# Kernel tuning notes

Hardware: AMD Instinct MI355X
Metric: run time of the kernel (lower is better)

The kernel has to match this reference:

```python
import jax, jax.numpy as jnp
import numpy as np

TEMP = float(np.e)

def _normalize(v):
    n = jnp.linalg.norm(v, axis=-1, keepdims=True)
    return v / jnp.maximum(n, 1e-12)

def setup_inputs() -> dict:
    key = jax.random.key(0)
    ks = jax.random.split(key, 18)
    N, D, H, O, E = 8192, 1024, 2048, 1024, 8
    s = 0.02
    return {
        "x": jax.random.normal(ks[0], (N, D), jnp.float32),
        "gate_w": jax.random.normal(ks[1], (D, E), jnp.float32) * s,
        "gate_b": jnp.zeros((E,), jnp.float32),
        "ph_w1": jax.random.normal(ks[2], (D, 32), jnp.float32) * s,
        "ph_b1": jnp.zeros((32,), jnp.float32),
        "ph_w2": jax.random.normal(ks[3], (32, 16), jnp.float32) * s,
        "ph_b2": jnp.zeros((16,), jnp.float32),
        "cl_w1": jax.random.normal(ks[4], (D, 16), jnp.float32) * s,
        "cl_b1": jnp.zeros((16,), jnp.float32),
        "cl_w2": jax.random.normal(ks[5], (16, 1), jnp.float32) * s,
        "cl_b2": jnp.zeros((1,), jnp.float32),
        "sigs": jax.random.normal(ks[6], (E, 16), jnp.float32) * 0.1,
        "e_w1": jax.random.normal(ks[7], (E, D, H), jnp.float32) * s,
        "e_b1": jnp.zeros((E, H), jnp.float32),
        "e_w2": jax.random.normal(ks[8], (E, H, O), jnp.float32) * s,
        "e_b2": jnp.zeros((E, O), jnp.float32),
    }

def reference(x, gate_w, gate_b, ph_w1, ph_b1, ph_w2, ph_b2,
              cl_w1, cl_b1, cl_w2, cl_b2, sigs, e_w1, e_b1, e_w2, e_b2):
    E = sigs.shape[0]
    # gating
    scores = (x @ gate_w + gate_b) / TEMP            # [N, E]
    probs = jax.nn.softmax(scores, axis=-1)
    # ph signature matching
    ph_feat = _normalize(jax.nn.relu(x @ ph_w1 + ph_b1) @ ph_w2 + ph_b2)  # [N, 16]
    sig_n = _normalize(sigs)                          # [E, 16]
    ph_match = (ph_feat @ sig_n.T + 1.0) / 2.0        # [N, E]
    effective = probs * ph_match
    # data-dependent k (torch uses .item(); here traced int used only in mask compare)
    clarity = jax.nn.sigmoid(jax.nn.relu(x @ cl_w1 + cl_b1) @ cl_w2 + cl_b2)  # [N,1]
    n_active = E - clarity[:, 0] * (E - 2)
    k = jnp.clip(jnp.floor(n_active.mean() + 0.5).astype(jnp.int32), 2, E)
    # rank-based top-k mask (jit-compatible for traced k)
    ranks = jnp.argsort(jnp.argsort(-effective, axis=-1), axis=-1)  # [N, E]
    mask = (ranks < k).astype(effective.dtype)
    weights = effective * mask
    weights = weights / (weights.sum(axis=-1, keepdims=True) + 1e-8)
    # load-balance loss
    f = (weights > 0).astype(probs.dtype).mean(axis=0)
    P = probs.mean(axis=0)
    lb_loss = 0.01 * E * (f * P).sum()
    # dense all-expert MLP (dropout is identity at eval)
    h = jax.nn.relu(jnp.einsum('nd,edh->neh', x, e_w1) + e_b1)   # [N, E, H]
    outs = jnp.einsum('neh,eho->neo', h, e_w2) + e_b2            # [N, E, O]
    y = jnp.einsum('ne,neo->no', weights, outs)                   # [N, O]
    return y, lb_loss
```

## Files before the change

kernel.cpp:

```cpp
#include <hip/hip_runtime.h>
#include <hip/hip_bf16.h>
#include <stdint.h>

typedef __attribute__((ext_vector_type(8))) _Float16 half8;
typedef __attribute__((ext_vector_type(4))) float f32x4;
typedef __attribute__((ext_vector_type(4))) unsigned short us4;
typedef __attribute__((ext_vector_type(8))) unsigned short us8;
typedef __attribute__((ext_vector_type(4))) int i32x4;

#define N_TOK 8192
#define DIM   1024
#define HDIM  2048
#define ODIM  1024

__device__ __forceinline__ unsigned short f2h(float f) {
  _Float16 h = (_Float16)f;
  union { _Float16 h; unsigned short u; } c; c.h = h; return c.u;
}

__device__ __forceinline__ void gload_lds16(const void* g, void* l) {
  __builtin_amdgcn_global_load_lds(
      (const __attribute__((address_space(1))) unsigned int*)g,
      (__attribute__((address_space(3))) unsigned int*)l, 16, 0, 0);
}

template <int EPI>
__global__ __launch_bounds__(256) void gemm_kernel(
    const unsigned short* __restrict__ A, const unsigned short* __restrict__ B,
    int N, int K,
    const float* __restrict__ bias, unsigned short* __restrict__ Hout,
    const float* __restrict__ Wg, int e, float* __restrict__ Y,
    const int* __restrict__ lst, const int* __restrict__ cntTrue,
    const int* __restrict__ cntPad)
{
  __shared__ half8 ldsA[2][512];
  __shared__ half8 ldsB[2][512];
  const int lane = threadIdx.x & 63, wid = threadIdx.x >> 6;
  const int wr = wid >> 1, wc = wid & 1;

  const int nwg = gridDim.x * gridDim.y;
  const int orig = blockIdx.y * gridDim.x + blockIdx.x;
  const int qq = nwg >> 3;
  const int swz = (orig & 7) * qq + (orig >> 3);
  const int bx = swz % gridDim.x, by = swz / gridDim.x;
  const int rowbase = by * 128, colbase = bx * 128;

  const int padc = cntPad[e];
  if (rowbase >= padc) return;

  int rG0 = rowbase + lane, rG1 = rowbase + 64 + lane;
  if (EPI == 1) { rG0 = lst[rG0]; rG1 = lst[rG1]; }

  f32x4 acc[4][4];
#pragma unroll
  for (int m = 0; m < 4; ++m)
#pragma unroll
    for (int n = 0; n < 4; ++n) acc[m][n] = f32x4{0.f, 0.f, 0.f, 0.f};

  auto stage = [&](int buf, int ktile) {
#pragma unroll
    for (int i = 0; i < 4; ++i) {
      const int c = wid * 4 + i;
      const int cc = c & 7, kq = cc >> 1, half = cc & 1;
      const int koff = ktile * 32 + kq * 8;
      if (c < 8) {
        const int arow = half ? rG1 : rG0;
        gload_lds16(A + (size_t)arow * K + koff,
                    &ldsA[buf][kq * 128 + half * 64]);
      } else {
        gload_lds16(B + (size_t)(colbase + half * 64 + lane) * K + koff,
                    &ldsB[buf][kq * 128 + half * 64]);
      }
    }
  };

  const int KT = K >> 5;
  stage(0, 0);
  for (int kt = 0; kt < KT; ++kt) {
    const int buf = kt & 1;
    __syncthreads();
    if (kt + 1 < KT) stage(buf ^ 1, kt + 1);

    half8 af[4], bfr[4];
    const int kqo = (lane >> 4) * 128;
    const int rA = wr * 64 + (lane & 15);
    const int rB = wc * 64 + (lane & 15);
#pragma unroll
    for (int m = 0; m < 4; ++m) af[m] = ldsA[buf][kqo + rA + m * 16];
#pragma unroll
    for (int n = 0; n < 4; ++n) bfr[n] = ldsB[buf][kqo + rB + n * 16];
#pragma unroll
    for (int m = 0; m < 4; ++m)
#pragma unroll
      for (int n = 0; n < 4; ++n)
        acc[m][n] = __builtin_amdgcn_mfma_f32_16x16x32_f16(af[m], bfr[n], acc[m][n], 0, 0, 0);
  }

  const int r0 = rowbase + wr * 64, c0 = colbase + wc * 64;
  if (EPI == 1) {
#pragma unroll
    for (int n = 0; n < 4; ++n) {
      const int col = c0 + n * 16 + (lane & 15);
      const float bv = bias[col];
#pragma unroll
      for (int m = 0; m < 4; ++m)
#pragma unroll
        for (int r = 0; r < 4; ++r) {
          const int slot = r0 + m * 16 + (lane >> 4) * 4 + r;
          float v = acc[m][n][r] + bv;
          v = v > 0.f ? v : 0.f;
          Hout[(size_t)slot * N + col] = f2h(v);
        }
    }
  } else {
    const int cntT = cntTrue[e];
#pragma unroll
    for (int m = 0; m < 4; ++m) {
      const int sbase = r0 + m * 16 + (lane >> 4) * 4;
      const i32x4 og = *(const i32x4*)&lst[sbase];
#pragma unroll
      for (int r = 0; r < 4; ++r) {
        const int slot = sbase + r;
        if (slot < cntT) {
          const int otok = og[r];
          const float wv = Wg[otok * 8 + e];
#pragma unroll
          for (int n = 0; n < 4; ++n) {
            const int col = c0 + n * 16 + (lane & 15);
            Y[(size_t)otok * ODIM + col] += wv * acc[m][n][r];
          }
        }
      }
    }
  }
}

__global__ __launch_bounds__(256) void gating_kernel(
    const float* __restrict__ x,
    const float* __restrict__ gate_w, const float* __restrict__ gate_b,
    const float* __restrict__ ph_w1, const float* __restrict__ ph_b1,
    const float* __restrict__ ph_w2, const float* __restrict__ ph_b2,
    const float* __restrict__ cl_w1, const float* __restrict__ cl_b1,
    const float* __restrict__ cl_w2, const float* __restrict__ cl_b2,
    const float* __restrict__ sigs,
    unsigned short* __restrict__ xh,
    float* __restrict__ eff_o,
    float* __restrict__ pclar, float* __restrict__ pP)
{
  const int lane = threadIdx.x & 63, wid = threadIdx.x >> 6;
  const int tok = blockIdx.x * 4 + wid;

  float g[8], p1[32], c1[16];
#pragma unroll
  for (int i = 0; i < 8; ++i) g[i] = 0.f;
#pragma unroll
  for (int i = 0; i < 32; ++i) p1[i] = 0.f;
#pragma unroll
  for (int i = 0; i < 16; ++i) c1[i] = 0.f;

  const f32x4* x4 = (const f32x4*)(x + (size_t)tok * DIM);
  us4* xh4 = (us4*)(xh + (size_t)tok * DIM);
#pragma unroll
  for (int d0 = 0; d0 < 4; ++d0) {
    const f32x4 xv = x4[d0 * 64 + lane];
    us4 ov;
#pragma unroll
    for (int j = 0; j < 4; ++j) {
      const int d = (d0 * 64 + lane) * 4 + j;
      const float xd = xv[j];
      ov[j] = f2h(xd);
      const f32x4* gw = (const f32x4*)(gate_w + d * 8);
#pragma unroll
      for (int q = 0; q < 2; ++q) { const f32x4 w = gw[q];
#pragma unroll
        for (int r = 0; r < 4; ++r) g[q * 4 + r] += xd * w[r]; }
      const f32x4* pw = (const f32x4*)(ph_w1 + d * 32);
#pragma unroll
      for (int q = 0; q < 8; ++q) { const f32x4 w = pw[q];
#pragma unroll
        for (int r = 0; r < 4; ++r) p1[q * 4 + r] += xd * w[r]; }
      const f32x4* cw = (const f32x4*)(cl_w1 + d * 16);
#pragma unroll
      for (int q = 0; q < 4; ++q) { const f32x4 w = cw[q];
#pragma unroll
        for (int r = 0; r < 4; ++r) c1[q * 4 + r] += xd * w[r]; }
    }
    xh4[d0 * 64 + lane] = ov;
  }
#pragma unroll
  for (int i = 0; i < 8; ++i)
#pragma unroll
    for (int s = 0; s < 6; ++s) g[i] += __shfl_xor(g[i], 1 << s);
#pragma unroll
  for (int i = 0; i < 32; ++i)
#pragma unroll
    for (int s = 0; s < 6; ++s) p1[i] += __shfl_xor(p1[i], 1 << s);
#pragma unroll
  for (int i = 0; i < 16; ++i)
#pragma unroll
    for (int s = 0; s < 6; ++s) c1[i] += __shfl_xor(c1[i], 1 << s);

  float sc[8]; float mx = -1e30f;
#pragma unroll
  for (int k = 0; k < 8; ++k) { sc[k] = (g[k] + gate_b[k]) / 2.718281828459045f; mx = fmaxf(mx, sc[k]); }
  float ex[8]; float sum = 0.f;
#pragma unroll
  for (int k = 0; k < 8; ++k) { ex[k] = expf(sc[k] - mx); sum += ex[k]; }
  float pe[8];
#pragma unroll
  for (int k = 0; k < 8; ++k) pe[k] = ex[k] / sum;

  float rh[32];
#pragma unroll
  for (int h = 0; h < 32; ++h) { const float v = p1[h] + ph_b1[h]; rh[h] = v > 0.f ? v : 0.f; }
  float feat[16];
#pragma unroll
  for (int q = 0; q < 16; ++q) {
    float f = ph_b2[q];
#pragma unroll
    for (int h = 0; h < 32; ++h) f += rh[h] * ph_w2[h * 16 + q];
    feat[q] = f;
  }
  float nn = 0.f;
#pragma unroll
  for (int q = 0; q < 16; ++q) nn += feat[q] * feat[q];
  const float den = fmaxf(sqrtf(nn), 1e-12f);
#pragma unroll
  for (int q = 0; q < 16; ++q) feat[q] = feat[q] / den;

  float eff[8];
#pragma unroll
  for (int k = 0; k < 8; ++k) {
    float s2 = 0.f;
#pragma unroll
    for (int q = 0; q < 16; ++q) { const float sv = sigs[k * 16 + q]; s2 += sv * sv; }
    const float sden = fmaxf(sqrtf(s2), 1e-12f);
    float dot = 0.f;
#pragma unroll
    for (int q = 0; q < 16; ++q) dot += feat[q] * (sigs[k * 16 + q] / sden);
    eff[k] = pe[k] * ((dot + 1.0f) / 2.0f);
  }

  float z = cl_b2[0];
#pragma unroll
  for (int c = 0; c < 16; ++c) { float v = c1[c] + cl_b1[c]; v = v > 0.f ? v : 0.f; z += v * cl_w2[c]; }
  const float clar = 1.0f / (1.0f + expf(-z));

  if (lane == 0) {
#pragma unroll
    for (int k = 0; k < 8; ++k) eff_o[tok * 8 + k] = eff[k];
  }
  __shared__ float shc[4];
  __shared__ float shP[4][8];
  if (lane == 0) { shc[wid] = clar;
#pragma unroll
    for (int k = 0; k < 8; ++k) shP[wid][k] = pe[k]; }
  __syncthreads();
  if (threadIdx.x == 0) {
    pclar[blockIdx.x] = shc[0] + shc[1] + shc[2] + shc[3];
#pragma unroll
    for (int k = 0; k < 8; ++k)
      pP[blockIdx.x * 8 + k] = shP[0][k] + shP[1][k] + shP[2][k] + shP[3][k];
  }
}

__global__ void zero_kernel(int* __restrict__ gcount) {
  if (threadIdx.x < 8) gcount[threadIdx.x] = 0;
}

__global__ __launch_bounds__(256) void weights_kernel(
    const float* __restrict__ eff_i, const float* __restrict__ pclar,
    float* __restrict__ wout, int* __restrict__ f_part,
    int* __restrict__ gcount, int* __restrict__ lst)
{
  __shared__ float red[256];
  __shared__ int cnt[8];
  __shared__ int ksh;
  const int tid = threadIdx.x;
  float s = 0.f;
  for (int i = tid; i < 2048; i += 256) s += pclar[i];
  red[tid] = s; __syncthreads();
  for (int off = 128; off > 0; off >>= 1) { if (tid < off) red[tid] += red[tid + off]; __syncthreads(); }
  if (tid == 0) {
    const float mean_na = 8.0f - 6.0f * (red[0] / 8192.0f);
    int k = (int)floorf(mean_na + 0.5f);
    ksh = k < 2 ? 2 : (k > 8 ? 8 : k);
  }
  if (tid < 8) cnt[tid] = 0;
  __syncthreads();
  const int k = ksh;
  const int t = blockIdx.x * 256 + tid;
  const f32x4* ep = (const f32x4*)(eff_i + t * 8);
  const f32x4 ea = ep[0], eb = ep[1];
  const float ef[8] = {ea[0], ea[1], ea[2], ea[3], eb[0], eb[1], eb[2], eb[3]};
  float w[8]; float wsum = 0.f; int act[8];
#pragma unroll
  for (int e2 = 0; e2 < 8; ++e2) {
    int r = 0;
#pragma unroll
    for (int j = 0; j < 8; ++j) r += (int)((ef[j] > ef[e2]) || ((j < e2) && (ef[j] == ef[e2])));
    const float we = (r < k) ? ef[e2] : 0.f;
    w[e2] = we; wsum += we; act[e2] = we > 0.f ? 1 : 0;
  }
  const float dn = wsum + 1e-8f;
#pragma unroll
  for (int e2 = 0; e2 < 8; ++e2) wout[t * 8 + e2] = w[e2] / dn;
#pragma unroll
  for (int e2 = 0; e2 < 8; ++e2)
    if (act[e2]) {
      atomicAdd(&cnt[e2], 1);
      const int p = atomicAdd(&gcount[e2], 1);
      lst[e2 * N_TOK + p] = t;
    }
  __syncthreads();
  if (tid < 8) f_part[blockIdx.x * 8 + tid] = cnt[tid];
}

__global__ __launch_bounds__(256) void pad_kernel(
    const int* __restrict__ gcount, int* __restrict__ gpad, int* __restrict__ lst)
{
  const int tid = threadIdx.x;
  for (int e2 = 0; e2 < 8; ++e2) {
    const int a = gcount[e2];
    const int pc = (a + 127) & ~127;
    if (tid == 0) gpad[e2] = pc;
    if (a > 0) {
      const int last = lst[e2 * N_TOK + a - 1];
      for (int i = a + tid; i < pc; i += 256) lst[e2 * N_TOK + i] = last;
    }
  }
}

__global__ __launch_bounds__(256) void lb_kernel(
    const float* __restrict__ pP, const int* __restrict__ f_part, float* __restrict__ lbout)
{
  __shared__ float red[256];
  __shared__ float Ps[8], Fs[8];
  const int tid = threadIdx.x;
  for (int e2 = 0; e2 < 8; ++e2) {
    float s = 0.f;
    for (int i = tid; i < 2048; i += 256) s += pP[i * 8 + e2];
    red[tid] = s; __syncthreads();
    for (int off = 128; off > 0; off >>= 1) { if (tid < off) red[tid] += red[tid + off]; __syncthreads(); }
    if (tid == 0) Ps[e2] = red[0];
    __syncthreads();
    red[tid] = (tid < 32) ? (float)f_part[tid * 8 + e2] : 0.f;
    __syncthreads();
    for (int off = 128; off > 0; off >>= 1) { if (tid < off) red[tid] += red[tid + off]; __syncthreads(); }
    if (tid == 0) Fs[e2] = red[0];
    __syncthreads();
  }
  if (tid == 0) {
    float lb = 0.f;
    for (int e2 = 0; e2 < 8; ++e2) lb += (Fs[e2] / 8192.0f) * (Ps[e2] / 8192.0f);
    lbout[0] = 0.01f * 8.0f * lb;
  }
}

__global__ __launch_bounds__(256) void yinit_kernel(
    const float* __restrict__ w, const float* __restrict__ b2, float* __restrict__ y)
{
  const int idx = blockIdx.x * 256 + threadIdx.x;
  const int n = idx >> 8, o4 = idx & 255;
  const f32x4* bv = (const f32x4*)b2;
  f32x4 a = f32x4{0.f, 0.f, 0.f, 0.f};
  const float* wr = w + n * 8;
#pragma unroll
  for (int e2 = 0; e2 < 8; ++e2) a += wr[e2] * bv[e2 * 256 + o4];
  ((f32x4*)y)[idx] = a;
}

__global__ __launch_bounds__(256) void transpose_kernel(
    const float* __restrict__ in, unsigned short* __restrict__ out, int R, int C)
{
  __shared__ __align__(16) unsigned short tb[64][72];
  const float* ip = in + (size_t)blockIdx.z * R * C;
  unsigned short* op = out + (size_t)blockIdx.z * R * C;
  const int r0 = blockIdx.y * 64, c0 = blockIdx.x * 64;
  const int tr = threadIdx.x >> 4, tc4 = (threadIdx.x & 15) * 4;
#pragma unroll
  for (int i = 0; i < 4; ++i) {
    const int rr = tr + i * 16;
    const f32x4 v = *(const f32x4*)(ip + (size_t)(r0 + rr) * C + c0 + tc4);
#pragma unroll
    for (int j = 0; j < 4; ++j) tb[tc4 + j][rr] = f2h(v[j]);
  }
  __syncthreads();
  const int oc = threadIdx.x >> 3, or8 = (threadIdx.x & 7) * 8;
#pragma unroll
  for (int i = 0; i < 2; ++i) {
    const int c = oc + i * 32;
    const us8 v = *(const us8*)&tb[c][or8];
    *(us8*)(op + (size_t)(c0 + c) * R + r0 + or8) = v;
  }
}

extern "C" void kernel_launch(void* const* d_in, const int* in_sizes, int n_in,
                              void* d_out, int out_size, void* d_ws, size_t ws_size,
                              hipStream_t stream)
{
  const float* x      = (const float*)d_in[0];
  const float* gate_w = (const float*)d_in[1];
  const float* gate_b = (const float*)d_in[2];
  const float* ph_w1  = (const float*)d_in[3];
  const float* ph_b1  = (const float*)d_in[4];
  const float* ph_w2  = (const float*)d_in[5];
  const float* ph_b2  = (const float*)d_in[6];
  const float* cl_w1  = (const float*)d_in[7];
  const float* cl_b1  = (const float*)d_in[8];
  const float* cl_w2  = (const float*)d_in[9];
  const float* cl_b2  = (const float*)d_in[10];
  const float* sigs   = (const float*)d_in[11];
  const float* e_w1   = (const float*)d_in[12];
  const float* e_b1   = (const float*)d_in[13];
  const float* e_w2   = (const float*)d_in[14];
  const float* e_b2   = (const float*)d_in[15];
  float* y = (float*)d_out;
  char* ws = (char*)d_ws;

  float* eff    = (float*)(ws + 0);
  float* wts    = (float*)(ws + 262144);
  float* pclar  = (float*)(ws + 524288);
  float* pP     = (float*)(ws + 532480);
  int*   f_part = (int*)(ws + 598016);
  int*   gcount = (int*)(ws + 599040);
  int*   gpad   = (int*)(ws + 599072);
  int*   lst    = (int*)(ws + 655360);
  unsigned short* xh  = (unsigned short*)(ws + 1048576);
  unsigned short* W1T = (unsigned short*)(ws + 17825792u);
  unsigned short* W2T = (unsigned short*)(ws + 51380224u);
  unsigned short* Hh  = (unsigned short*)(ws + 84934656u);

  transpose_kernel<<<dim3(32, 16, 8), 256, 0, stream>>>(e_w1, W1T, 1024, 2048);
  transpose_kernel<<<dim3(16, 32, 8), 256, 0, stream>>>(e_w2, W2T, 2048, 1024);
  gating_kernel<<<2048, 256, 0, stream>>>(x, gate_w, gate_b, ph_w1, ph_b1, ph_w2, ph_b2,
                                          cl_w1, cl_b1, cl_w2, cl_b2, sigs,
                                          xh, eff, pclar, pP);
  zero_kernel<<<1, 64, 0, stream>>>(gcount);
  weights_kernel<<<32, 256, 0, stream>>>(eff, pclar, wts, f_part, gcount, lst);
  pad_kernel<<<1, 256, 0, stream>>>(gcount, gpad, lst);
  lb_kernel<<<1, 256, 0, stream>>>(pP, f_part, y + (size_t)N_TOK * ODIM);
  yinit_kernel<<<8192, 256, 0, stream>>>(wts, e_b2, y);

  for (int e2 = 0; e2 < 8; ++e2) {
    gemm_kernel<1><<<dim3(16, 64), 256, 0, stream>>>(
        xh, W1T + (size_t)e2 * HDIM * DIM, HDIM, DIM,
        e_b1 + e2 * HDIM, Hh, nullptr, e2, nullptr,
        lst + (size_t)e2 * N_TOK, gcount, gpad);
    gemm_kernel<2><<<dim3(8, 64), 256, 0, stream>>>(
        Hh, W2T + (size_t)e2 * ODIM * HDIM, ODIM, HDIM,
        nullptr, nullptr, wts, e2, y,
        lst + (size_t)e2 * N_TOK, gcount, gpad);
  }
}
```

Measured before the change: 1.977 ms.

## Restructure gating projections to stage weights in LDS and parallelize over outputs

The gating kernel used to have each lane hold 56 accumulators over a slice of D, then reduce them with 336 cross-lane shuffles per wave. Now each block stages 128-row chunks of the concatenated gate/ph/cl weights in shared memory. Each lane computes one of the 56 output columns over the full D, reading x from LDS. This removes the heavy shuffle reduction and register pressure and shares weight loads across the 4 tokens in a block. The cost is extra __syncthreads per chunk, and only half the lanes load x, which may reduce memory parallelism.

After: 1.892 ms. 1.05x faster.

```diff
diff --git a/kernel.cpp b/kernel.cpp
--- a/kernel.cpp
+++ b/kernel.cpp
@@ -147,72 +147,79 @@
     float* __restrict__ eff_o,
     float* __restrict__ pclar, float* __restrict__ pP)
 {
-  const int lane = threadIdx.x & 63, wid = threadIdx.x >> 6;
+  __shared__ float Wl[128][60];
+  __shared__ float xs[4][128];
+  __shared__ float sS[4][56];
+  __shared__ float shc[4];
+  __shared__ float shP[4][8];
+
+  const int t = threadIdx.x;
+  const int lane = t & 63, wid = t >> 6;
   const int tok = blockIdx.x * 4 + wid;
-
-  float g[8], p1[32], c1[16];
-#pragma unroll
-  for (int i = 0; i < 8; ++i) g[i] = 0.f;
-#pragma unroll
-  for (int i = 0; i < 32; ++i) p1[i] = 0.f;
-#pragma unroll
-  for (int i = 0; i < 16; ++i) c1[i] = 0.f;
+  const int o = lane < 56 ? lane : lane - 56;
 
   const f32x4* x4 = (const f32x4*)(x + (size_t)tok * DIM);
   us4* xh4 = (us4*)(xh + (size_t)tok * DIM);
-#pragma unroll
-  for (int d0 = 0; d0 < 4; ++d0) {
-    const f32x4 xv = x4[d0 * 64 + lane];
-    us4 ov;
-#pragma unroll
-    for (int j = 0; j < 4; ++j) {
-      const int d = (d0 * 64 + lane) * 4 + j;
-      const float xd = xv[j];
-      ov[j] = f2h(xd);
-      const f32x4* gw = (const f32x4*)(gate_w + d * 8);
-#pragma unroll
-      for (int q = 0; q < 2; ++q) { const f32x4 w = gw[q];
-#pragma unroll
-        for (int r = 0; r < 4; ++r) g[q * 4 + r] += xd * w[r]; }
-      const f32x4* pw = (const f32x4*)(ph_w1 + d * 32);
-#pragma unroll
-      for (int q = 0; q < 8; ++q) { const f32x4 w = pw[q];
-#pragma unroll
-        for (int r = 0; r < 4; ++r) p1[q * 4 + r] += xd * w[r]; }
-      const f32x4* cw = (const f32x4*)(cl_w1 + d * 16);
-#pragma unroll
-      for (int q = 0; q < 4; ++q) { const f32x4 w = cw[q];
-#pragma unroll
-        for (int r = 0; r < 4; ++r) c1[q * 4 + r] += xd * w[r]; }
-    }
-    xh4[d0 * 64 + lane] = ov;
-  }
-#pragma unroll
-  for (int i = 0; i < 8; ++i)
-#pragma unroll
-    for (int s = 0; s < 6; ++s) g[i] += __shfl_xor(g[i], 1 << s);
-#pragma unroll
-  for (int i = 0; i < 32; ++i)
-#pragma unroll
-    for (int s = 0; s < 6; ++s) p1[i] += __shfl_xor(p1[i], 1 << s);
-#pragma unroll
-  for (int i = 0; i < 16; ++i)
-#pragma unroll
-    for (int s = 0; s < 6; ++s) c1[i] += __shfl_xor(c1[i], 1 << s);
+
+  float acc = 0.f;
+
+#pragma unroll 1
+  for (int c = 0; c < 8; ++c) {
+    __syncthreads();
+    if (t < 128) {
+      const int gr = c * 128 + t;
+      const float* grow = gate_w + (size_t)gr * 8;
+      *(f32x4*)&Wl[t][0] = *(const f32x4*)(grow);
+      *(f32x4*)&Wl[t][4] = *(const f32x4*)(grow + 4);
+      const float* prow = ph_w1 + (size_t)gr * 32;
+#pragma unroll
+      for (int q = 0; q < 8; ++q)
+        *(f32x4*)&Wl[t][8 + 4 * q] = *(const f32x4*)(prow + 4 * q);
+      const float* crow = cl_w1 + (size_t)gr * 16;
+#pragma unroll
+      for (int q = 0; q < 4; ++q)
+        *(f32x4*)&Wl[t][40 + 4 * q] = *(const f32x4*)(crow + 4 * q);
+    }
+    if (lane < 32) {
+      const int l32 = lane;
+      const f32x4 xv = x4[c * 32 + l32];
+      us4 ov;
+#pragma unroll
+      for (int j = 0; j < 4; ++j) ov[j] = f2h(xv[j]);
+      xh4[c * 32 + l32] = ov;
+      *(f32x4*)&xs[wid][l32 * 4] = xv;
+    }
+    __syncthreads();
+
+#pragma unroll
+    for (int i4 = 0; i4 < 32; ++i4) {
+      const f32x4 xq = *(const f32x4*)&xs[wid][i4 * 4];
+      acc += xq[0] * Wl[i4 * 4 + 0][o];
+      acc += xq[1] * Wl[i4 * 4 + 1][o];
+      acc += xq[2] * Wl[i4 * 4 + 2][o];
+      acc += xq[3] * Wl[i4 * 4 + 3][o];
+    }
+  }
+
+  if (lane < 56) sS[wid][lane] = acc;
+  __syncthreads();
+
+  float S[56];
+#pragma unroll
+  for (int q = 0; q < 56; ++q) S[q] = sS[wid][q];
 
   float sc[8]; float mx = -1e30f;
 #pragma unroll
-  for (int k = 0; k < 8; ++k) { sc[k] = (g[k] + gate_b[k]) / 2.718281828459045f; mx = fmaxf(mx, sc[k]); }
-  float ex[8]; float sum = 0.f;
-#pragma unroll
-  for (int k = 0; k < 8; ++k) { ex[k] = expf(sc[k] - mx); sum += ex[k]; }
-  float pe[8];
-#pragma unroll
-  for (int k = 0; k < 8; ++k) pe[k] = ex[k] / sum;
+  for (int k = 0; k < 8; ++k) { sc[k] = (S[k] + gate_b[k]) / 2.718281828459045f; mx = fmaxf(mx, sc[k]); }
+  float sum = 0.f; float pe[8];
+#pragma unroll
+  for (int k = 0; k < 8; ++k) { pe[k] = expf(sc[k] - mx); sum += pe[k]; }
+#pragma unroll
+  for (int k = 0; k < 8; ++k) pe[k] /= sum;
 
   float rh[32];
 #pragma unroll
-  for (int h = 0; h < 32; ++h) { const float v = p1[h] + ph_b1[h]; rh[h] = v > 0.f ? v : 0.f; }
+  for (int h = 0; h < 32; ++h) { const float v = S[8 + h] + ph_b1[h]; rh[h] = v > 0.f ? v : 0.f; }
   float feat[16];
 #pragma unroll
   for (int q = 0; q < 16; ++q) {
@@ -226,7 +233,7 @@
   for (int q = 0; q < 16; ++q) nn += feat[q] * feat[q];
   const float den = fmaxf(sqrtf(nn), 1e-12f);
 #pragma unroll
-  for (int q = 0; q < 16; ++q) feat[q] = feat[q] / den;
+  for (int q = 0; q < 16; ++q) feat[q] /= den;
 
   float eff[8];
 #pragma unroll
@@ -243,20 +250,18 @@
 
   float z = cl_b2[0];
 #pragma unroll
-  for (int c = 0; c < 16; ++c) { float v = c1[c] + cl_b1[c]; v = v > 0.f ? v : 0.f; z += v * cl_w2[c]; }
+  for (int cc = 0; cc < 16; ++cc) { float v = S[40 + cc] + cl_b1[cc]; v = v > 0.f ? v : 0.f; z += v * cl_w2[cc]; }
   const float clar = 1.0f / (1.0f + expf(-z));
 
   if (lane == 0) {
 #pragma unroll
     for (int k = 0; k < 8; ++k) eff_o[tok * 8 + k] = eff[k];
-  }
-  __shared__ float shc[4];
-  __shared__ float shP[4][8];
-  if (lane == 0) { shc[wid] = clar;
-#pragma unroll
-    for (int k = 0; k < 8; ++k) shP[wid][k] = pe[k]; }
+    shc[wid] = clar;
+#pragma unroll
+    for (int k = 0; k < 8; ++k) shP[wid][k] = pe[k];
+  }
   __syncthreads();
-  if (threadIdx.x == 0) {
+  if (t == 0) {
     pclar[blockIdx.x] = shc[0] + shc[1] + shc[2] + shc[3];
 #pragma unroll
     for (int k = 0; k < 8; ++k)
```
